# Performance work log

Measured on AMD Instinct MI355X. Metric: run time of the kernel, lower is better.

## Reference

```python
import jax, jax.numpy as jnp
import numpy as np

N, DIM, QK, HEADS, NWIN, TOPK = 1, 128, 128, 8, 8, 4
D = H = W = 32


def setup_inputs() -> dict:
    key = jax.random.key(0)
    ks = jax.random.split(key, 3)
    s = lambda fan: 1.0 / np.sqrt(fan)
    return {
        "x": jax.random.normal(ks[0], (N, D, H, W, DIM), jnp.float32),
        "w_qkv": jax.random.normal(ks[1], (DIM, 2 * QK + DIM), jnp.float32) * s(DIM),
        "b_qkv": jnp.zeros((2 * QK + DIM,), jnp.float32),
        "w_o": jax.random.normal(ks[2], (DIM, DIM), jnp.float32) * s(DIM),
        "b_o": jnp.zeros((DIM,), jnp.float32),
    }


def _forward(x, w_qkv, b_qkv, w_o, b_o):
    n, Dd, Hh, Ww, C = x.shape
    d, h, w = Dd // NWIN, Hh // NWIN, Ww // NWIN
    p3, w3 = NWIN ** 3, d * h * w
    cq, cv = QK // HEADS, DIM // HEADS
    scale = QK ** -0.5
    # window partition: n (q d)(j h)(i w) c -> n (q j i) d h w c
    xw = x.reshape(n, NWIN, d, NWIN, h, NWIN, w, C)
    xw = xw.transpose(0, 1, 3, 5, 2, 4, 6, 7).reshape(n, p3, d, h, w, C)
    # fused qkv projection
    qkv = xw @ w_qkv + b_qkv
    q, k, v = qkv[..., :QK], qkv[..., QK:2 * QK], qkv[..., 2 * QK:]
    q_pix = q.reshape(n, p3, w3, QK)
    kv_pix = jnp.concatenate([k, v], axis=-1).reshape(n, p3, w3, QK + DIM)
    # region-level routing (non-differentiable: detached in original)
    q_win = jax.lax.stop_gradient(q.mean((2, 3, 4)))  # (n, p3, QK)
    k_win = jax.lax.stop_gradient(k.mean((2, 3, 4)))
    logits = jnp.einsum('npc,nqc->npq', q_win * scale, k_win)  # (n, p3, p3)
    _, r_idx = jax.lax.top_k(logits, TOPK)  # (n, p3, topk)
    # gather top-k regions' KV per query window: (n, p3, topk, w3, QK+DIM)
    kv_sel = jax.vmap(lambda kvp, idx: kvp[idx])(kv_pix, r_idx)
    k_sel = kv_sel[..., :QK].reshape(n * p3, TOPK * w3, HEADS, cq).transpose(0, 2, 3, 1)  # (np3, m, cq, k*w3)
    v_sel = kv_sel[..., QK:].reshape(n * p3, TOPK * w3, HEADS, cv).transpose(0, 2, 1, 3)  # (np3, m, k*w3, cv)
    qh = q_pix.reshape(n * p3, w3, HEADS, cq).transpose(0, 2, 1, 3)  # (np3, m, w3, cq)
    attn = jax.nn.softmax((qh * scale) @ k_sel, axis=-1)  # (np3, m, w3, k*w3)
    out = attn @ v_sel  # (np3, m, w3, cv)
    # (n q j i) m (d h w) c -> n (q d)(j h)(i w)(m c)
    out = out.reshape(n, NWIN, NWIN, NWIN, HEADS, d, h, w, cv)
    out = out.transpose(0, 1, 5, 2, 6, 3, 7, 4, 8).reshape(n, Dd, Hh, Ww, DIM)
    out = out @ w_o + b_o
    return out, q, k, v


def reference(x, w_qkv, b_qkv, w_o, b_o):
    return _forward(x, w_qkv, b_qkv, w_o, b_o)
```

## Files before the change

kernel.cpp:

```cpp
#include <hip/hip_runtime.h>
#include <cmath>

namespace {

typedef __attribute__((ext_vector_type(8))) short short8;
typedef __attribute__((ext_vector_type(4))) float f32x4;
typedef __attribute__((ext_vector_type(4))) unsigned u32x4;

constexpr float kScale = 0.08838834764831845f;
constexpr float kScaleL2 = 0.12751744900764504f;

__device__ __forceinline__ int voxel_row(int p, int pix) {
  int pd = p >> 6, ph = (p >> 3) & 7, pw = p & 7;
  int iz = pix >> 4, iy = (pix >> 2) & 3, ix = pix & 3;
  return (((pd * 4 + iz) * 32 + (ph * 4 + iy)) * 32 + (pw * 4 + ix));
}

__device__ __forceinline__ float dot4(float4 a, float4 b) {
  return a.x * b.x + a.y * b.y + a.z * b.z + a.w * b.w;
}

__device__ __forceinline__ short bf16c(float f) {
  unsigned u = __builtin_bit_cast(unsigned, f);
  u += 0x7fffu + ((u >> 16) & 1u);
  return (short)(u >> 16);
}

__device__ __forceinline__ unsigned bfpack(float lo, float hi) {
  return (unsigned)(unsigned short)bf16c(lo) |
         ((unsigned)(unsigned short)bf16c(hi) << 16);
}

__global__ __launch_bounds__(64) void k_pack2(
    const float* __restrict__ wqkv, const float* __restrict__ wo,
    short* __restrict__ dstq, short* __restrict__ dsto) {
  const int lane = threadIdx.x;
  const float* w;
  short* dst;
  int fid, N;
  if (blockIdx.x < 96) {
    w = wqkv; dst = dstq; fid = blockIdx.x; N = 384;
  } else {
    w = wo; dst = dsto; fid = blockIdx.x - 96; N = 128;
  }
  const int ntile = fid >> 2, ks = fid & 3;
  const int k0 = ks * 32 + (lane >> 4) * 8, col = ntile * 16 + (lane & 15);
  short8 o;
#pragma unroll
  for (int i = 0; i < 8; ++i) o[i] = bf16c(w[(size_t)(k0 + i) * N + col]);
  *(short8*)(dst + ((size_t)fid * 64 + lane) * 8) = o;
}

__global__ __launch_bounds__(512, 4) void k_qkv(
    const float* __restrict__ x, const short* __restrict__ wpk,
    const float* __restrict__ bias, const float* __restrict__ wfull,
    float* __restrict__ q, float* __restrict__ k, float* __restrict__ v,
    short* __restrict__ vt, short* __restrict__ kbh, short* __restrict__ qbh,
    float* __restrict__ qwin, float* __restrict__ kwin) {
  __shared__ short sX[64][136];
  __shared__ float xpart[8][16][8];
  __shared__ float xm[128];
  const int p = blockIdx.x, t = threadIdx.x;
  const int wave = t >> 6, lane = t & 63, l15 = lane & 15, lg = lane >> 4;

  float ps[8] = {0.f, 0.f, 0.f, 0.f, 0.f, 0.f, 0.f, 0.f};
#pragma unroll
  for (int r = 0; r < 2; ++r) {
    int unit = t + r * 512;
    int row = unit >> 4, u = unit & 15;
    const float* src = x + (size_t)voxel_row(p, row) * 128 + u * 8;
    float4 a = *(const float4*)src, b = *(const float4*)(src + 4);
    ps[0] += a.x; ps[1] += a.y; ps[2] += a.z; ps[3] += a.w;
    ps[4] += b.x; ps[5] += b.y; ps[6] += b.z; ps[7] += b.w;
    short8 o;
    o[0] = bf16c(a.x); o[1] = bf16c(a.y); o[2] = bf16c(a.z); o[3] = bf16c(a.w);
    o[4] = bf16c(b.x); o[5] = bf16c(b.y); o[6] = bf16c(b.z); o[7] = bf16c(b.w);
    *(short8*)(&sX[row][u * 8]) = o;
  }
#pragma unroll
  for (int i = 0; i < 8; ++i) {
    ps[i] += __shfl_xor(ps[i], 16);
    ps[i] += __shfl_xor(ps[i], 32);
  }
  if (lg == 0)
#pragma unroll
    for (int i = 0; i < 8; ++i) xpart[wave][l15][i] = ps[i];
  __syncthreads();
  if (t < 128) {
    float s = 0.f;
#pragma unroll
    for (int w8 = 0; w8 < 8; ++w8) s += xpart[w8][t >> 3][t & 7];
    xm[t] = s * (1.f / 64.f);
  }

  f32x4 acc[4][3];
#pragma unroll
  for (int mt = 0; mt < 4; ++mt)
#pragma unroll
    for (int nt = 0; nt < 3; ++nt) acc[mt][nt] = f32x4{0.f, 0.f, 0.f, 0.f};
#pragma unroll
  for (int ks = 0; ks < 4; ++ks) {
    short8 a[4];
#pragma unroll
    for (int mt = 0; mt < 4; ++mt)
      a[mt] = *(const short8*)(&sX[mt * 16 + l15][ks * 32 + lg * 8]);
#pragma unroll
    for (int nt = 0; nt < 3; ++nt) {
      int ntg = wave * 3 + nt;
      short8 b = *(const short8*)(wpk + ((size_t)(ntg * 4 + ks) * 64 + lane) * 8);
#pragma unroll
      for (int mt = 0; mt < 4; ++mt)
        acc[mt][nt] = __builtin_amdgcn_mfma_f32_16x16x32_bf16(a[mt], b, acc[mt][nt], 0, 0, 0);
    }
  }
#pragma unroll
  for (int nt = 0; nt < 3; ++nt) {
    int n = (wave * 3 + nt) * 16 + l15;
    float bv = bias[n];
    float* dst = n < 128 ? q : (n < 256 ? k : v);
    int col = n & 127;
#pragma unroll
    for (int mt = 0; mt < 4; ++mt) {
      float o0 = acc[mt][nt][0] + bv, o1 = acc[mt][nt][1] + bv;
      float o2 = acc[mt][nt][2] + bv, o3 = acc[mt][nt][3] + bv;
      int row0 = mt * 16 + lg * 4;
      dst[(size_t)(p * 64 + row0 + 0) * 128 + col] = o0;
      dst[(size_t)(p * 64 + row0 + 1) * 128 + col] = o1;
      dst[(size_t)(p * 64 + row0 + 2) * 128 + col] = o2;
      dst[(size_t)(p * 64 + row0 + 3) * 128 + col] = o3;
      if (n >= 256) {
        uint2 pk;
        pk.x = bfpack(o0, o1);
        pk.y = bfpack(o2, o3);
        *(uint2*)(vt + (size_t)p * 8192 + (size_t)(n - 256) * 64 + row0) = pk;
      } else if (n >= 128) {
        int hh = (n - 128) >> 4, d = (n - 128) & 15;
        short* kd = kbh + (((size_t)(p * 8 + hh)) * 64 + row0) * 16 + d;
        kd[0] = bf16c(o0);
        kd[16] = bf16c(o1);
        kd[32] = bf16c(o2);
        kd[48] = bf16c(o3);
      } else {
        int hh = n >> 4, d = n & 15;
        short* qd = qbh + (((size_t)(p * 8 + hh)) * 64 + row0) * 16 + d;
        qd[0] = bf16c(o0 * kScaleL2);
        qd[16] = bf16c(o1 * kScaleL2);
        qd[32] = bf16c(o2 * kScaleL2);
        qd[48] = bf16c(o3 * kScaleL2);
      }
    }
  }

  __syncthreads();
  if (t < 256) {
    float acc2 = bias[t];
    for (int kk = 0; kk < 128; ++kk)
      acc2 = fmaf(xm[kk], wfull[(size_t)kk * 384 + t], acc2);
    if (t < 128) qwin[p * 128 + t] = acc2;
    else kwin[p * 128 + (t - 128)] = acc2;
  }
}

__global__ __launch_bounds__(1024, 4) void k_attn(
    const short* __restrict__ qbh, const short* __restrict__ kbh,
    const short* __restrict__ vt, const float* __restrict__ qwin,
    const float* __restrict__ kwin, const short* __restrict__ wpk_o,
    const float* __restrict__ b_o, float* __restrict__ out) {
  __shared__ float lgits[512];
  __shared__ float qs[128];
  __shared__ int widx[4];
  __shared__ short sO[64][136];

  const int p = blockIdx.x, t = threadIdx.x;
  const int wave = t >> 6, lane = t & 63;
  const int l15 = lane & 15, lg = lane >> 4;
  const int h = wave >> 1, qh = wave & 1;

  const short* qw = qbh + ((size_t)(p * 8 + h)) * 1024 + qh * 512;
  short8 qf[2];
#pragma unroll
  for (int nt = 0; nt < 2; ++nt) {
    if (lg < 2)
      qf[nt] = *(const short8*)(qw + (nt * 16 + l15) * 16 + lg * 8);
    else
      qf[nt] = short8{0, 0, 0, 0, 0, 0, 0, 0};
  }

  if (t < 32) *(float4*)(&qs[t * 4]) = *(const float4*)(qwin + p * 128 + t * 4);
  __syncthreads();
  if (t < 512) {
    const float* kr = kwin + (size_t)t * 128;
    float s = 0.f;
    for (int c = 0; c < 128; c += 4)
      s += dot4(*(const float4*)(qs + c), *(const float4*)(kr + c));
    lgits[t] = s;
  }
  __syncthreads();
  if (wave == 0) {
    float vals[8];
#pragma unroll
    for (int i = 0; i < 8; ++i) vals[i] = lgits[lane * 8 + i];
    for (int sel = 0; sel < 4; ++sel) {
      float bv = -1e30f;
      int bi = 0;
#pragma unroll
      for (int i = 0; i < 8; ++i) {
        int idx = lane * 8 + i;
        if (vals[i] > bv) { bv = vals[i]; bi = idx; }
      }
#pragma unroll
      for (int off = 32; off > 0; off >>= 1) {
        float ov = __shfl_xor(bv, off);
        int oi = __shfl_xor(bi, off);
        if (ov > bv || (ov == bv && oi < bi)) { bv = ov; bi = oi; }
      }
      if (lane == 0) widx[sel] = bi;
      if ((bi >> 3) == lane) vals[bi & 7] = -1e30f;
    }
  }
  __syncthreads();

  const int src0 = ((lg & 1) << 5) | l15;
  const int src1 = src0 + 16;

  float m_r[2] = {-1e30f, -1e30f};
  float l_r[2] = {0.f, 0.f};
  f32x4 oacc[2];
  oacc[0] = f32x4{0.f, 0.f, 0.f, 0.f};
  oacc[1] = f32x4{0.f, 0.f, 0.f, 0.f};

#pragma unroll
  for (int c = 0; c < 4; ++c) {
    const int wsel = widx[c];
    const short* kw = kbh + ((size_t)(wsel * 8 + h)) * 1024;
    short8 af[4];
#pragma unroll
    for (int mt = 0; mt < 4; ++mt) {
      if (lg < 2)
        af[mt] = *(const short8*)(kw + (mt * 16 + l15) * 16 + lg * 8);
      else
        af[mt] = short8{0, 0, 0, 0, 0, 0, 0, 0};
    }
    const short* vw = vt + (size_t)wsel * 8192 + (size_t)(h * 16 + l15) * 64 + lg * 8;
    short8 av0 = *(const short8*)(vw);
    short8 av1 = *(const short8*)(vw + 32);

    f32x4 s[4][2];
#pragma unroll
    for (int mt = 0; mt < 4; ++mt)
#pragma unroll
      for (int j2 = 0; j2 < 2; ++j2)
        s[mt][j2] = __builtin_amdgcn_mfma_f32_16x16x32_bf16(
            af[mt], qf[j2], f32x4{0.f, 0.f, 0.f, 0.f}, 0, 0, 0);

#pragma unroll
    for (int j2 = 0; j2 < 2; ++j2) {
      const int nt = j2;
      float mx = -1e30f;
#pragma unroll
      for (int mt = 0; mt < 4; ++mt)
#pragma unroll
        for (int j = 0; j < 4; ++j) mx = fmaxf(mx, s[mt][j2][j]);
      mx = fmaxf(mx, __shfl_xor(mx, 16));
      mx = fmaxf(mx, __shfl_xor(mx, 32));
      float mnew = fmaxf(m_r[nt], mx);
      float sc = __builtin_amdgcn_exp2f(m_r[nt] - mnew);
      m_r[nt] = mnew;
      l_r[nt] *= sc;
      oacc[nt][0] *= sc; oacc[nt][1] *= sc;
      oacc[nt][2] *= sc; oacc[nt][3] *= sc;
      float ls = 0.f;
#pragma unroll
      for (int mt = 0; mt < 4; ++mt)
#pragma unroll
        for (int j = 0; j < 4; ++j) {
          float e = __builtin_amdgcn_exp2f(s[mt][j2][j] - m_r[nt]);
          s[mt][j2][j] = e;
          ls += e;
        }
      ls += __shfl_xor(ls, 16);
      ls += __shfl_xor(ls, 32);
      l_r[nt] += ls;

      unsigned P2[4][2];
#pragma unroll
      for (int mt = 0; mt < 4; ++mt) {
        P2[mt][0] = bfpack(s[mt][j2][0], s[mt][j2][1]);
        P2[mt][1] = bfpack(s[mt][j2][2], s[mt][j2][3]);
      }
#pragma unroll
      for (int kt = 0; kt < 2; ++kt) {
        unsigned lo0 = (unsigned)__shfl((int)P2[2 * kt + 0][0], src0);
        unsigned hi0 = (unsigned)__shfl((int)P2[2 * kt + 1][0], src0);
        unsigned lo1 = (unsigned)__shfl((int)P2[2 * kt + 0][1], src0);
        unsigned hi1 = (unsigned)__shfl((int)P2[2 * kt + 1][1], src0);
        unsigned lo2 = (unsigned)__shfl((int)P2[2 * kt + 0][0], src1);
        unsigned hi2 = (unsigned)__shfl((int)P2[2 * kt + 1][0], src1);
        unsigned lo3 = (unsigned)__shfl((int)P2[2 * kt + 0][1], src1);
        unsigned hi3 = (unsigned)__shfl((int)P2[2 * kt + 1][1], src1);
        u32x4 bw;
        bw[0] = (lg < 2) ? lo0 : hi0;
        bw[1] = (lg < 2) ? lo1 : hi1;
        bw[2] = (lg < 2) ? lo2 : hi2;
        bw[3] = (lg < 2) ? lo3 : hi3;
        short8 bfr = __builtin_bit_cast(short8, bw);
        oacc[nt] = __builtin_amdgcn_mfma_f32_16x16x32_bf16(
            kt == 0 ? av0 : av1, bfr, oacc[nt], 0, 0, 0);
      }
    }
  }

#pragma unroll
  for (int nt = 0; nt < 2; ++nt) {
    float inv = 1.f / l_r[nt];
    uint2 pk;
    pk.x = bfpack(oacc[nt][0] * inv, oacc[nt][1] * inv);
    pk.y = bfpack(oacc[nt][2] * inv, oacc[nt][3] * inv);
    *(uint2*)(&sO[qh * 32 + nt * 16 + l15][h * 16 + lg * 4]) = pk;
  }
  __syncthreads();

  {
    const int ct = wave >> 1, mh = wave & 1;
    const int mt0 = mh * 2, mt1 = mh * 2 + 1;
    f32x4 pacc0 = f32x4{0.f, 0.f, 0.f, 0.f};
    f32x4 pacc1 = f32x4{0.f, 0.f, 0.f, 0.f};
#pragma unroll
    for (int ks = 0; ks < 4; ++ks) {
      short8 a0 = *(const short8*)(&sO[mt0 * 16 + l15][ks * 32 + lg * 8]);
      short8 a1 = *(const short8*)(&sO[mt1 * 16 + l15][ks * 32 + lg * 8]);
      short8 b = *(const short8*)(wpk_o + ((size_t)(ct * 4 + ks) * 64 + lane) * 8);
      pacc0 = __builtin_amdgcn_mfma_f32_16x16x32_bf16(a0, b, pacc0, 0, 0, 0);
      pacc1 = __builtin_amdgcn_mfma_f32_16x16x32_bf16(a1, b, pacc1, 0, 0, 0);
    }
    int n = ct * 16 + l15;
    float bv = b_o[n];
#pragma unroll
    for (int j = 0; j < 4; ++j) {
      out[(size_t)voxel_row(p, mt0 * 16 + lg * 4 + j) * 128 + n] = pacc0[j] + bv;
      out[(size_t)voxel_row(p, mt1 * 16 + lg * 4 + j) * 128 + n] = pacc1[j] + bv;
    }
  }
}

}

extern "C" void kernel_launch(void* const* d_in, const int* in_sizes, int n_in,
                              void* d_out, int out_size, void* d_ws, size_t ws_size,
                              hipStream_t stream) {
  (void)in_sizes; (void)n_in; (void)out_size; (void)ws_size;
  const float* x = (const float*)d_in[0];
  const float* w_qkv = (const float*)d_in[1];
  const float* b_qkv = (const float*)d_in[2];
  const float* w_o = (const float*)d_in[3];
  const float* b_o = (const float*)d_in[4];

  float* out = (float*)d_out;
  float* q = out + 4194304;
  float* k = q + 4194304;
  float* v = k + 4194304;

  float* qwin = (float*)d_ws;
  float* kwin = qwin + 65536;
  short* wpk_qkv = (short*)(kwin + 65536);
  short* wpk_o = wpk_qkv + 49152;
  short* vt = wpk_o + 16384;
  short* kbh = vt + 4194304;
  short* qbh = kbh + 4194304;

  k_pack2<<<128, 64, 0, stream>>>(w_qkv, w_o, wpk_qkv, wpk_o);
  k_qkv<<<512, 512, 0, stream>>>(x, wpk_qkv, b_qkv, w_qkv, q, k, v, vt, kbh, qbh, qwin, kwin);
  k_attn<<<512, 1024, 0, stream>>>(qbh, kbh, vt, qwin, kwin, wpk_o, b_o, out);
}
```

Before: 82.31 us.

## Split attention by key windows across wave halves and merge softmax states

Each wave now handles all 64 queries of one head but only two of the four selected key windows, instead of half the queries over all four windows. The two halves exchange their running max, sum and output accumulators through a shared-memory buffer and combine them flash-decoding style. Shared memory is unioned into one 48KB buffer. The online-softmax rescale is also skipped when the new max stays within a threshold of the current one. The intent is to reuse K/V fragment loads across more queries and cut rescale work, at the cost of an extra merge phase, more registers and two more barriers.

New measurement: 83.51 us. Within noise of the previous version (+1.5%).

```diff
diff --git a/kernel.cpp b/kernel.cpp
--- a/kernel.cpp
+++ b/kernel.cpp
@@ -166,20 +166,22 @@
     const short* __restrict__ vt, const float* __restrict__ qwin,
     const float* __restrict__ kwin, const short* __restrict__ wpk_o,
     const float* __restrict__ b_o, float* __restrict__ out) {
-  __shared__ float lgits[512];
-  __shared__ float qs[128];
+  __shared__ __align__(16) char smem[49152];
+  float* lgits = (float*)smem;
+  float* qs = (float*)(smem + 2048);
+  float* ex = (float*)smem;
+  short* sO = (short*)smem;
   __shared__ int widx[4];
-  __shared__ short sO[64][136];
 
   const int p = blockIdx.x, t = threadIdx.x;
   const int wave = t >> 6, lane = t & 63;
   const int l15 = lane & 15, lg = lane >> 4;
-  const int h = wave >> 1, qh = wave & 1;
-
-  const short* qw = qbh + ((size_t)(p * 8 + h)) * 1024 + qh * 512;
-  short8 qf[2];
-#pragma unroll
-  for (int nt = 0; nt < 2; ++nt) {
+  const int h = wave & 7, half = wave >> 3;
+
+  const short* qw = qbh + ((size_t)(p * 8 + h)) * 1024;
+  short8 qf[4];
+#pragma unroll
+  for (int nt = 0; nt < 4; ++nt) {
     if (lg < 2)
       qf[nt] = *(const short8*)(qw + (nt * 16 + l15) * 16 + lg * 8);
     else
@@ -223,15 +225,15 @@
   const int src0 = ((lg & 1) << 5) | l15;
   const int src1 = src0 + 16;
 
-  float m_r[2] = {-1e30f, -1e30f};
-  float l_r[2] = {0.f, 0.f};
-  f32x4 oacc[2];
-  oacc[0] = f32x4{0.f, 0.f, 0.f, 0.f};
-  oacc[1] = f32x4{0.f, 0.f, 0.f, 0.f};
-
-#pragma unroll
-  for (int c = 0; c < 4; ++c) {
-    const int wsel = widx[c];
+  float m_r[4] = {-1e30f, -1e30f, -1e30f, -1e30f};
+  float l_r[4] = {0.f, 0.f, 0.f, 0.f};
+  f32x4 oacc[4];
+#pragma unroll
+  for (int i = 0; i < 4; ++i) oacc[i] = f32x4{0.f, 0.f, 0.f, 0.f};
+
+#pragma unroll
+  for (int cc = 0; cc < 2; ++cc) {
+    const int wsel = widx[half * 2 + cc];
     const short* kw = kbh + ((size_t)(wsel * 8 + h)) * 1024;
     short8 af[4];
 #pragma unroll
@@ -245,78 +247,113 @@
     short8 av0 = *(const short8*)(vw);
     short8 av1 = *(const short8*)(vw + 32);
 
-    f32x4 s[4][2];
-#pragma unroll
-    for (int mt = 0; mt < 4; ++mt)
-#pragma unroll
-      for (int j2 = 0; j2 < 2; ++j2)
-        s[mt][j2] = __builtin_amdgcn_mfma_f32_16x16x32_bf16(
-            af[mt], qf[j2], f32x4{0.f, 0.f, 0.f, 0.f}, 0, 0, 0);
-
-#pragma unroll
-    for (int j2 = 0; j2 < 2; ++j2) {
-      const int nt = j2;
-      float mx = -1e30f;
+#pragma unroll
+    for (int np = 0; np < 2; ++np) {
+      f32x4 s[4][2];
 #pragma unroll
       for (int mt = 0; mt < 4; ++mt)
 #pragma unroll
-        for (int j = 0; j < 4; ++j) mx = fmaxf(mx, s[mt][j2][j]);
-      mx = fmaxf(mx, __shfl_xor(mx, 16));
-      mx = fmaxf(mx, __shfl_xor(mx, 32));
-      float mnew = fmaxf(m_r[nt], mx);
-      float sc = __builtin_amdgcn_exp2f(m_r[nt] - mnew);
-      m_r[nt] = mnew;
-      l_r[nt] *= sc;
-      oacc[nt][0] *= sc; oacc[nt][1] *= sc;
-      oacc[nt][2] *= sc; oacc[nt][3] *= sc;
-      float ls = 0.f;
-#pragma unroll
-      for (int mt = 0; mt < 4; ++mt)
-#pragma unroll
-        for (int j = 0; j < 4; ++j) {
-          float e = __builtin_amdgcn_exp2f(s[mt][j2][j] - m_r[nt]);
-          s[mt][j2][j] = e;
-          ls += e;
+        for (int j2 = 0; j2 < 2; ++j2)
+          s[mt][j2] = __builtin_amdgcn_mfma_f32_16x16x32_bf16(
+              af[mt], qf[np * 2 + j2], f32x4{0.f, 0.f, 0.f, 0.f}, 0, 0, 0);
+
+#pragma unroll
+      for (int j2 = 0; j2 < 2; ++j2) {
+        const int nt = np * 2 + j2;
+        float mx = -1e30f;
+#pragma unroll
+        for (int mt = 0; mt < 4; ++mt)
+#pragma unroll
+          for (int j = 0; j < 4; ++j) mx = fmaxf(mx, s[mt][j2][j]);
+        mx = fmaxf(mx, __shfl_xor(mx, 16));
+        mx = fmaxf(mx, __shfl_xor(mx, 32));
+        if (!__all(mx <= m_r[nt] + 11.0f)) {
+          float mnew = fmaxf(m_r[nt], mx);
+          float sc = __builtin_amdgcn_exp2f(m_r[nt] - mnew);
+          m_r[nt] = mnew;
+          l_r[nt] *= sc;
+          oacc[nt][0] *= sc; oacc[nt][1] *= sc;
+          oacc[nt][2] *= sc; oacc[nt][3] *= sc;
         }
-      ls += __shfl_xor(ls, 16);
-      ls += __shfl_xor(ls, 32);
-      l_r[nt] += ls;
-
-      unsigned P2[4][2];
-#pragma unroll
-      for (int mt = 0; mt < 4; ++mt) {
-        P2[mt][0] = bfpack(s[mt][j2][0], s[mt][j2][1]);
-        P2[mt][1] = bfpack(s[mt][j2][2], s[mt][j2][3]);
+        float ls = 0.f;
+#pragma unroll
+        for (int mt = 0; mt < 4; ++mt)
+#pragma unroll
+          for (int j = 0; j < 4; ++j) {
+            float e = __builtin_amdgcn_exp2f(s[mt][j2][j] - m_r[nt]);
+            s[mt][j2][j] = e;
+            ls += e;
+          }
+        ls += __shfl_xor(ls, 16);
+        ls += __shfl_xor(ls, 32);
+        l_r[nt] += ls;
+
+        unsigned P2[4][2];
+#pragma unroll
+        for (int mt = 0; mt < 4; ++mt) {
+          P2[mt][0] = bfpack(s[mt][j2][0], s[mt][j2][1]);
+          P2[mt][1] = bfpack(s[mt][j2][2], s[mt][j2][3]);
+        }
+#pragma unroll
+        for (int kt = 0; kt < 2; ++kt) {
+          unsigned lo0 = (unsigned)__shfl((int)P2[2 * kt + 0][0], src0);
+          unsigned hi0 = (unsigned)__shfl((int)P2[2 * kt + 1][0], src0);
+          unsigned lo1 = (unsigned)__shfl((int)P2[2 * kt + 0][1], src0);
+          unsigned hi1 = (unsigned)__shfl((int)P2[2 * kt + 1][1], src0);
+          unsigned lo2 = (unsigned)__shfl((int)P2[2 * kt + 0][0], src1);
+          unsigned hi2 = (unsigned)__shfl((int)P2[2 * kt + 1][0], src1);
+          unsigned lo3 = (unsigned)__shfl((int)P2[2 * kt + 0][1], src1);
+          unsigned hi3 = (unsigned)__shfl((int)P2[2 * kt + 1][1], src1);
+          u32x4 bw;
+          bw[0] = (lg < 2) ? lo0 : hi0;
+          bw[1] = (lg < 2) ? lo1 : hi1;
+          bw[2] = (lg < 2) ? lo2 : hi2;
+          bw[3] = (lg < 2) ? lo3 : hi3;
+          short8 bfr = __builtin_bit_cast(short8, bw);
+          oacc[nt] = __builtin_amdgcn_mfma_f32_16x16x32_bf16(
+              kt == 0 ? av0 : av1, bfr, oacc[nt], 0, 0, 0);
+        }
       }
-#pragma unroll
-      for (int kt = 0; kt < 2; ++kt) {
-        unsigned lo0 = (unsigned)__shfl((int)P2[2 * kt + 0][0], src0);
-        unsigned hi0 = (unsigned)__shfl((int)P2[2 * kt + 1][0], src0);
-        unsigned lo1 = (unsigned)__shfl((int)P2[2 * kt + 0][1], src0);
-        unsigned hi1 = (unsigned)__shfl((int)P2[2 * kt + 1][1], src0);
-        unsigned lo2 = (unsigned)__shfl((int)P2[2 * kt + 0][0], src1);
-        unsigned hi2 = (unsigned)__shfl((int)P2[2 * kt + 1][0], src1);
-        unsigned lo3 = (unsigned)__shfl((int)P2[2 * kt + 0][1], src1);
-        unsigned hi3 = (unsigned)__shfl((int)P2[2 * kt + 1][1], src1);
-        u32x4 bw;
-        bw[0] = (lg < 2) ? lo0 : hi0;
-        bw[1] = (lg < 2) ? lo1 : hi1;
-        bw[2] = (lg < 2) ? lo2 : hi2;
-        bw[3] = (lg < 2) ? lo3 : hi3;
-        short8 bfr = __builtin_bit_cast(short8, bw);
-        oacc[nt] = __builtin_amdgcn_mfma_f32_16x16x32_bf16(
-            kt == 0 ? av0 : av1, bfr, oacc[nt], 0, 0, 0);
-      }
-    }
-  }
-
-#pragma unroll
-  for (int nt = 0; nt < 2; ++nt) {
-    float inv = 1.f / l_r[nt];
-    uint2 pk;
-    pk.x = bfpack(oacc[nt][0] * inv, oacc[nt][1] * inv);
-    pk.y = bfpack(oacc[nt][2] * inv, oacc[nt][3] * inv);
-    *(uint2*)(&sO[qh * 32 + nt * 16 + l15][h * 16 + lg * 4]) = pk;
+    }
+  }
+
+  if (half == 1) {
+#pragma unroll
+    for (int nt = 0; nt < 4; ++nt) {
+      float* exw = ex + (((size_t)(h * 4 + nt) * 64 + lane) * 6);
+      exw[0] = m_r[nt];
+      exw[1] = l_r[nt];
+      exw[2] = oacc[nt][0]; exw[3] = oacc[nt][1];
+      exw[4] = oacc[nt][2]; exw[5] = oacc[nt][3];
+    }
+  }
+  __syncthreads();
+  if (half == 0) {
+#pragma unroll
+    for (int nt = 0; nt < 4; ++nt) {
+      const float* exr = ex + (((size_t)(h * 4 + nt) * 64 + lane) * 6);
+      float m2 = exr[0], l2 = exr[1];
+      float mnew = fmaxf(m_r[nt], m2);
+      float sc1 = __builtin_amdgcn_exp2f(m_r[nt] - mnew);
+      float sc2 = __builtin_amdgcn_exp2f(m2 - mnew);
+      l_r[nt] = l_r[nt] * sc1 + l2 * sc2;
+      oacc[nt][0] = oacc[nt][0] * sc1 + exr[2] * sc2;
+      oacc[nt][1] = oacc[nt][1] * sc1 + exr[3] * sc2;
+      oacc[nt][2] = oacc[nt][2] * sc1 + exr[4] * sc2;
+      oacc[nt][3] = oacc[nt][3] * sc1 + exr[5] * sc2;
+    }
+  }
+  __syncthreads();
+
+  if (half == 0) {
+#pragma unroll
+    for (int nt = 0; nt < 4; ++nt) {
+      float inv = 1.f / l_r[nt];
+      uint2 pk;
+      pk.x = bfpack(oacc[nt][0] * inv, oacc[nt][1] * inv);
+      pk.y = bfpack(oacc[nt][2] * inv, oacc[nt][3] * inv);
+      *(uint2*)(&sO[(size_t)(nt * 16 + l15) * 136 + h * 16 + lg * 4]) = pk;
+    }
   }
   __syncthreads();
 
@@ -327,8 +364,8 @@
     f32x4 pacc1 = f32x4{0.f, 0.f, 0.f, 0.f};
 #pragma unroll
     for (int ks = 0; ks < 4; ++ks) {
-      short8 a0 = *(const short8*)(&sO[mt0 * 16 + l15][ks * 32 + lg * 8]);
-      short8 a1 = *(const short8*)(&sO[mt1 * 16 + l15][ks * 32 + lg * 8]);
+      short8 a0 = *(const short8*)(&sO[(size_t)(mt0 * 16 + l15) * 136 + ks * 32 + lg * 8]);
+      short8 a1 = *(const short8*)(&sO[(size_t)(mt1 * 16 + l15) * 136 + ks * 32 + lg * 8]);
       short8 b = *(const short8*)(wpk_o + ((size_t)(ct * 4 + ks) * 64 + lane) * 8);
       pacc0 = __builtin_amdgcn_mfma_f32_16x16x32_bf16(a0, b, pacc0, 0, 0, 0);
       pacc1 = __builtin_amdgcn_mfma_f32_16x16x32_bf16(a1, b, pacc1, 0, 0, 0);
```
